# Kernel optimization log

Measured on AMD Instinct MI355X. Metric: run time of the kernel, lower is better.

## Reference

```python
import jax, jax.numpy as jnp
import numpy as np

LAYER_SIZES = [256, 256, 256]
SPLIT_HALF = True
B, F0, D = 512, 32, 32


def setup_inputs() -> dict:
    key = jax.random.key(0)
    ks = jax.random.split(key, 7)
    field_nums = [F0]
    for i, s in enumerate(LAYER_SIZES):
        field_nums.append(s // 2 if (SPLIT_HALF and i != len(LAYER_SIZES) - 1) else (s // 2 if SPLIT_HALF else s))
    # field_nums = [32, 128, 128, 128] (last entry unused for weights)
    inp = {
        'feat': jax.random.normal(ks[0], (B, F0, D), dtype=jnp.float32),
        'W0': jax.random.normal(ks[1], (LAYER_SIZES[0], field_nums[0], F0), dtype=jnp.float32) * 0.05,
        'b0': jnp.zeros((LAYER_SIZES[0],), dtype=jnp.float32),
        'W1': jax.random.normal(ks[2], (LAYER_SIZES[1], field_nums[1], F0), dtype=jnp.float32) * 0.05,
        'b1': jnp.zeros((LAYER_SIZES[1],), dtype=jnp.float32),
        'W2': jax.random.normal(ks[3], (LAYER_SIZES[2], field_nums[2], F0), dtype=jnp.float32) * 0.05,
        'b2': jnp.zeros((LAYER_SIZES[2],), dtype=jnp.float32),
    }
    return inp


def _cin_layer(h, feat, W, b):
    # h: [B,H,D], feat: [B,F0,D], W: [K,H,F0], b: [K] -> out [B,K,D]
    # outer product per embedding dim, then 1x1 conv (full [H,F0] contraction)
    z = jnp.einsum('bid,bjd->bdij', h, feat)          # [B,D,H,F0]
    out = jnp.einsum('bdij,kij->bkd', z, W) + b[None, :, None]
    return jax.nn.relu(out)


def reference(feat, W0, b0, W1, b1, W2, b2):
    Ws = [W0, W1, W2]
    bs = [b0, b1, b2]
    h = feat
    p = []
    n_layers = len(LAYER_SIZES)
    for l, K in enumerate(LAYER_SIZES):
        out = _cin_layer(h, feat, Ws[l], bs[l])        # [B,K,D]
        if SPLIT_HALF and l != n_layers - 1:
            h = out[:, :K // 2, :]
            direct = out[:, K // 2:, :]
        else:
            direct = out
            h = out
        p.append(direct)
    return jnp.concatenate(p, axis=1).sum(-1)          # [B, sum of direct sizes]
```

## Files before the change

### kernel.cpp

```cpp
#include <hip/hip_runtime.h>
#include <hip/hip_fp16.h>
#include <stdint.h>


typedef _Float16 half8_t __attribute__((ext_vector_type(8)));
typedef float f32x4 __attribute__((ext_vector_type(4)));
typedef float f32x16 __attribute__((ext_vector_type(16)));
typedef uint32_t u32x4 __attribute__((ext_vector_type(4)));

union H8 {
  half8_t h;
  uint32_t u[4];
  u32x4 q;
};

#define AS1 __attribute__((address_space(1)))
#define AS3 __attribute__((address_space(3)))

static __device__ __forceinline__ uint32_t pkmul(uint32_t x, uint32_t y) {
  __half2 a = __builtin_bit_cast(__half2, x);
  __half2 b = __builtin_bit_cast(__half2, y);
  __half2 r = __hmul2(a, b);
  return __builtin_bit_cast(uint32_t, r);
}

static __device__ __forceinline__ uint32_t pack2h(float a, float b) {
  __half2 r = __floats2half2_rn(a, b);
  return __builtin_bit_cast(uint32_t, r);
}

__global__ void prep_kernel(const float* __restrict__ W0, const float* __restrict__ W1,
                            const float* __restrict__ W2, const float* __restrict__ feat,
                            uint16_t* __restrict__ Wt0, uint16_t* __restrict__ Wt1,
                            uint16_t* __restrict__ Wt2,
                            uint16_t* __restrict__ F16, uint32_t* __restrict__ hP0) {
  int blk = blockIdx.x;
  if (blk < 1152) {
    const float* W; uint16_t* Wt; int FLsh, base;
    if (blk < 128)      { W = W0; Wt = Wt0; FLsh = 5; base = 0; }
    else if (blk < 640) { W = W1; Wt = Wt1; FLsh = 7; base = 128; }
    else                { W = W2; Wt = Wt2; FLsh = 7; base = 640; }
    int idx4 = (blk - base) * 256 + threadIdx.x;
    int jg = idx4 & 3;
    int i = (idx4 >> 2) & ((1 << FLsh) - 1);
    int k = idx4 >> (2 + FLsh);
    const float* src = W + ((size_t)(k << FLsh) + i) * 32 + jg * 8;
    float4 x0 = *(const float4*)(src);
    float4 x1 = *(const float4*)(src + 4);
    u32x4 o;
    o[0] = pack2h(x0.x, x0.y);
    o[1] = pack2h(x0.z, x0.w);
    o[2] = pack2h(x1.x, x1.y);
    o[3] = pack2h(x1.z, x1.w);
    int kr = k & 15, kt = k >> 4;
    *(u32x4*)((uint32_t*)Wt + (((size_t)i * 16 + kt) * 64 + jg * 16 + kr) * 4) = o;
  } else {
    int m = (blk - 1152) * 256 + threadIdx.x;
    int b = m >> 5, d = m & 31;
    const float* fb = feat + (size_t)b * 1024 + d;
    uint16_t hs[32];
#pragma unroll
    for (int j = 0; j < 32; ++j)
      hs[j] = __half_as_ushort(__float2half(fb[j * 32]));
    int mb = m >> 5, ml = m & 31;
#pragma unroll
    for (int jp = 0; jp < 16; ++jp) {
      uint32_t pr = (uint32_t)hs[2 * jp] | ((uint32_t)hs[2 * jp + 1] << 16);
      hP0[((size_t)(mb * 4 + (jp >> 2)) * 4 + (jp & 3)) * 32 + ml] = pr;
    }
#pragma unroll
    for (int c = 0; c < 4; ++c) {
      u32x4 q;
      q[0] = (uint32_t)hs[c * 8 + 0] | ((uint32_t)hs[c * 8 + 1] << 16);
      q[1] = (uint32_t)hs[c * 8 + 2] | ((uint32_t)hs[c * 8 + 3] << 16);
      q[2] = (uint32_t)hs[c * 8 + 4] | ((uint32_t)hs[c * 8 + 5] << 16);
      q[3] = (uint32_t)hs[c * 8 + 6] | ((uint32_t)hs[c * 8 + 7] << 16);
      *(u32x4*)(F16 + (size_t)m * 32 + c * 8) = q;
    }
  }
}

template <int FL>
__global__ __launch_bounds__(256, 2) void gemm_cin(
    const uint32_t* __restrict__ hP,
    const uint16_t* __restrict__ wt,
    const uint16_t* __restrict__ f16m,
    const float* __restrict__ bias,
    uint32_t* __restrict__ houtP,
    float* __restrict__ outp,
    int obase, int klo) {
  constexpr int NCHK = FL / 8;
  constexpr int NCM = NCHK - 1;
  __shared__ __align__(16) char smem[49152];
  const int tid = threadIdx.x;
  const int lane = tid & 63, w = tid >> 6;
  const int l31 = lane & 31, l5 = lane >> 5;
  const int kg = blockIdx.x & 7, mgrp = blockIdx.x >> 3;
  const int mb0 = mgrp * 8 + w * 2;

  const uint16_t* fb0 = f16m + (size_t)(mb0 * 32 + l31) * 32 + l5 * 8;
  H8 ffA0, ffA1, ffB0, ffB1;
  ffA0.q = *(const u32x4*)(fb0);
  ffA1.q = *(const u32x4*)(fb0 + 16);
  ffB0.q = *(const u32x4*)(fb0 + 1024);
  ffB1.q = *(const u32x4*)(fb0 + 1040);

  const char* wsrc = (const char*)wt + kg * 2048 + (size_t)(tid >> 7) * 16384 +
                     (tid & 127) * 16;
  char* sdst = smem + tid * 16;

#define STAGE(QQ, BUFOFF)                                                     \
  { const char* s_ = wsrc + (size_t)((QQ) & NCM) * 131072;                    \
    char* d_ = sdst + (BUFOFF);                                               \
    _Pragma("unroll") for (int c_ = 0; c_ < 4; ++c_)                          \
      __builtin_amdgcn_global_load_lds(                                       \
          (const AS1 uint32_t*)(s_ + c_ * 32768),                             \
          (AS3 uint32_t*)(d_ + c_ * 4096), 16, 0, 0); }

  const uint32_t* hbA = hP + (size_t)mb0 * (FL / 8) * 128 + l31;
  const uint32_t* hbB = hbA + (size_t)(FL / 8) * 128;

#define HLD(QQ, DA, DB)                                                       \
  { const uint32_t* pa_ = hbA + ((QQ) & NCM) * 128;                           \
    const uint32_t* pb_ = hbB + ((QQ) & NCM) * 128;                           \
    DA[0] = pa_[0]; DA[1] = pa_[32]; DA[2] = pa_[64]; DA[3] = pa_[96];        \
    DB[0] = pb_[0]; DB[1] = pb_[32]; DB[2] = pb_[64]; DB[3] = pb_[96]; }

  u32x4 hcA, hcB, hnA, hnB;

  STAGE(0, 0)
  STAGE(1, 16384)
  HLD(0, hcA, hcB)

  f32x16 accA0 = {}, accA1 = {}, accB0 = {}, accB1 = {};
  const char* rbase = smem + ((l31 >> 4) << 10) + (l5 << 8) + ((lane & 15) << 4);

  asm volatile("s_waitcnt vmcnt(12)" ::: "memory");
  __builtin_amdgcn_s_barrier();

#define BSTEP(HA_, HB_, PSEL, BA0, BA1, BB0, BB1)                             \
  { uint32_t eA_ = __builtin_amdgcn_perm((HA_), (HA_), (PSEL));               \
    uint32_t eB_ = __builtin_amdgcn_perm((HB_), (HB_), (PSEL));               \
    _Pragma("unroll") for (int c_ = 0; c_ < 4; ++c_) {                        \
      BA0.u[c_] = pkmul(ffA0.u[c_], eA_);                                     \
      BA1.u[c_] = pkmul(ffA1.u[c_], eA_);                                     \
      BB0.u[c_] = pkmul(ffB0.u[c_], eB_);                                     \
      BB1.u[c_] = pkmul(ffB1.u[c_], eB_);                                     \
    } }

#define MQUAD(WE, WO, BA0, BA1, BB0, BB1)                                         \
  accA0 = __builtin_amdgcn_mfma_f32_32x32x16_f16((WE).h, BA0.h, accA0, 0, 0, 0);  \
  accB0 = __builtin_amdgcn_mfma_f32_32x32x16_f16((WE).h, BB0.h, accB0, 0, 0, 0);  \
  accA1 = __builtin_amdgcn_mfma_f32_32x32x16_f16((WO).h, BA1.h, accA1, 0, 0, 0);  \
  accB1 = __builtin_amdgcn_mfma_f32_32x32x16_f16((WO).h, BB1.h, accB1, 0, 0, 0);

#define CHUNK(QQ, RDOFF, STOFF, HCA_, HCB_, HNA_, HNB_)                           \
  { const char* rb_ = rbase + (RDOFF);                                            \
    H8 w0, w1, w2, w3, w4, w5, w6, w7, w8, w9, wa, wb, wc, wd, we, wf;            \
    w0.q = *(const u32x4*)(rb_ + 0 * 2048);                                       \
    w1.q = *(const u32x4*)(rb_ + 0 * 2048 + 512);                                 \
    w2.q = *(const u32x4*)(rb_ + 1 * 2048);                                       \
    w3.q = *(const u32x4*)(rb_ + 1 * 2048 + 512);                                 \
    w4.q = *(const u32x4*)(rb_ + 2 * 2048);                                       \
    w5.q = *(const u32x4*)(rb_ + 2 * 2048 + 512);                                 \
    w6.q = *(const u32x4*)(rb_ + 3 * 2048);                                       \
    w7.q = *(const u32x4*)(rb_ + 3 * 2048 + 512);                                 \
    w8.q = *(const u32x4*)(rb_ + 4 * 2048);                                       \
    w9.q = *(const u32x4*)(rb_ + 4 * 2048 + 512);                                 \
    wa.q = *(const u32x4*)(rb_ + 5 * 2048);                                       \
    wb.q = *(const u32x4*)(rb_ + 5 * 2048 + 512);                                 \
    wc.q = *(const u32x4*)(rb_ + 6 * 2048);                                       \
    wd.q = *(const u32x4*)(rb_ + 6 * 2048 + 512);                                 \
    we.q = *(const u32x4*)(rb_ + 7 * 2048);                                       \
    wf.q = *(const u32x4*)(rb_ + 7 * 2048 + 512);                                 \
    HLD((QQ) + 1, HNA_, HNB_)                                                     \
    STAGE((QQ) + 2, STOFF)                                                        \
               \
    { H8 pA0_0, pA1_0, pB0_0, pB1_0, pA0_1, pA1_1, pB0_1, pB1_1;                  \
      H8 pA0_2, pA1_2, pB0_2, pB1_2, pA0_3, pA1_3, pB0_3, pB1_3;                  \
      BSTEP(HCA_[0], HCB_[0], 0x01000100u, pA0_0, pA1_0, pB0_0, pB1_0)            \
      BSTEP(HCA_[0], HCB_[0], 0x03020302u, pA0_1, pA1_1, pB0_1, pB1_1)            \
      BSTEP(HCA_[1], HCB_[1], 0x01000100u, pA0_2, pA1_2, pB0_2, pB1_2)            \
      BSTEP(HCA_[1], HCB_[1], 0x03020302u, pA0_3, pA1_3, pB0_3, pB1_3)            \
      __builtin_amdgcn_s_setprio(1);                                              \
      MQUAD(w0, w1, pA0_0, pA1_0, pB0_0, pB1_0)                                   \
      MQUAD(w2, w3, pA0_1, pA1_1, pB0_1, pB1_1)                                   \
      MQUAD(w4, w5, pA0_2, pA1_2, pB0_2, pB1_2)                                   \
      MQUAD(w6, w7, pA0_3, pA1_3, pB0_3, pB1_3)                                   \
      __builtin_amdgcn_s_setprio(0); }                                            \
                                                          \
    { H8 pA0_0, pA1_0, pB0_0, pB1_0, pA0_1, pA1_1, pB0_1, pB1_1;                  \
      H8 pA0_2, pA1_2, pB0_2, pB1_2, pA0_3, pA1_3, pB0_3, pB1_3;                  \
      BSTEP(HCA_[2], HCB_[2], 0x01000100u, pA0_0, pA1_0, pB0_0, pB1_0)            \
      BSTEP(HCA_[2], HCB_[2], 0x03020302u, pA0_1, pA1_1, pB0_1, pB1_1)            \
      BSTEP(HCA_[3], HCB_[3], 0x01000100u, pA0_2, pA1_2, pB0_2, pB1_2)            \
      BSTEP(HCA_[3], HCB_[3], 0x03020302u, pA0_3, pA1_3, pB0_3, pB1_3)            \
      __builtin_amdgcn_s_setprio(1);                                              \
      MQUAD(w8, w9, pA0_0, pA1_0, pB0_0, pB1_0)                                   \
      MQUAD(wa, wb, pA0_1, pA1_1, pB0_1, pB1_1)                                   \
      MQUAD(wc, wd, pA0_2, pA1_2, pB0_2, pB1_2)                                   \
      MQUAD(we, wf, pA0_3, pA1_3, pB0_3, pB1_3)                                   \
      __builtin_amdgcn_s_setprio(0); }                                            \
    asm volatile("s_waitcnt vmcnt(12)" ::: "memory");                             \
    __builtin_amdgcn_s_barrier();                                                 \
  }

  int r0 = 0, r1 = 16384, r2 = 32768;
#pragma unroll 1
  for (int q = 0; q < NCHK; q += 2) {
    CHUNK(q, r0, r2, hcA, hcB, hnA, hnB)
    CHUNK(q + 1, r1, r0, hnA, hnB, hcA, hcB)
    int t = r2; r2 = r1; r1 = r0; r0 = t;
  }
#undef CHUNK
#undef MQUAD
#undef BSTEP
#undef STAGE
#undef HLD

  asm volatile("s_waitcnt vmcnt(0)" ::: "memory");

  f32x16 accA = accA0 + accA1;
  f32x16 accB = accB0 + accB1;
  f32x4 bv[4];
#pragma unroll
  for (int a = 0; a < 4; ++a)
    bv[a] = *(const f32x4*)(bias + kg * 32 + a * 8 + l5 * 4);

#define EPILOG(ACC, MB)                                                           \
  {                                                                               \
    float v[16];                                                                  \
    _Pragma("unroll") for (int a = 0; a < 4; ++a)                                 \
        _Pragma("unroll") for (int t = 0; t < 4; ++t) {                           \
      float x = ACC[a * 4 + t] + bv[a][t];                                        \
      v[a * 4 + t] = x > 0.f ? x : 0.f;                                           \
    }                                                                             \
    if (houtP != nullptr && kg < 4) {                                             \
      _Pragma("unroll") for (int a = 0; a < 4; ++a)                               \
          _Pragma("unroll") for (int c = 0; c < 2; ++c) {                         \
        uint32_t pr = pack2h(v[a * 4 + 2 * c], v[a * 4 + 2 * c + 1]);             \
        houtP[((size_t)((MB) * 16 + kg * 4 + a) * 4 + 2 * l5 + c) * 32 + l31] =   \
            pr;                                                                   \
      }                                                                           \
    }                                                                             \
    _Pragma("unroll") for (int r = 0; r < 16; ++r) {                              \
      float x = v[r];                                                             \
      x += __shfl_xor(x, 1); x += __shfl_xor(x, 2);                               \
      x += __shfl_xor(x, 4); x += __shfl_xor(x, 8);                               \
      x += __shfl_xor(x, 16);                                                     \
      v[r] = x;                                                                   \
    }                                                                             \
    if (kg * 32 >= klo && (lane == 0 || lane == 32)) {                            \
      float* ob = outp + (size_t)(MB) * 512 + obase + kg * 32 - klo + l5 * 4;     \
      _Pragma("unroll") for (int a = 0; a < 4; ++a)                               \
          *(f32x4*)(ob + a * 8) =                                                 \
              (f32x4){v[a * 4], v[a * 4 + 1], v[a * 4 + 2], v[a * 4 + 3]};        \
    }                                                                             \
  }

  EPILOG(accA, mb0)
  EPILOG(accB, mb0 + 1)
#undef EPILOG
}

extern "C" void kernel_launch(void* const* d_in, const int* in_sizes, int n_in,
                              void* d_out, int out_size, void* d_ws, size_t ws_size,
                              hipStream_t stream) {
  const float* feat = (const float*)d_in[0];
  const float* W0 = (const float*)d_in[1];
  const float* b0 = (const float*)d_in[2];
  const float* W1 = (const float*)d_in[3];
  const float* b1 = (const float*)d_in[4];
  const float* W2 = (const float*)d_in[5];
  const float* b2 = (const float*)d_in[6];
  float* out = (float*)d_out;
  char* ws = (char*)d_ws;

  uint16_t* Wt0 = (uint16_t*)(ws + 0x000000);
  uint16_t* Wt1 = (uint16_t*)(ws + 0x080000);
  uint16_t* Wt2 = (uint16_t*)(ws + 0x280000);
  uint16_t* F16 = (uint16_t*)(ws + 0x480000);
  uint32_t* hP0 = (uint32_t*)(ws + 0x580000);
  uint32_t* hP1 = (uint32_t*)(ws + 0x680000);
  uint32_t* hP2 = (uint32_t*)(ws + 0xA80000);

  prep_kernel<<<1216, 256, 0, stream>>>(W0, W1, W2, feat, Wt0, Wt1, Wt2, F16, hP0);

  gemm_cin<32><<<512, 256, 0, stream>>>(hP0, Wt0, F16, b0, hP1, out, 0, 128);
  gemm_cin<128><<<512, 256, 0, stream>>>(hP1, Wt1, F16, b1, hP2, out, 128, 128);
  gemm_cin<128><<<512, 256, 0, stream>>>(hP2, Wt2, F16, b2, (uint32_t*)nullptr,
                                         out, 256, 0);
}
```

Measured before the change: 107.7 us.

## Software-pipeline LDS weight reads and products across half-chunks with single accumulators

Restructures the main loop into a ping-pong schedule. Weight fragments for the next half-chunk are read from LDS, and the fp16 outer-product operands are computed, while MFMAs for the current half run. It also merges the even/odd accumulator pairs into one accumulator per batch row, which frees registers but lengthens MFMA dependency chains. Barriers and vmcnt waits are reordered (wait vmcnt(0) at start, vmcnt(20) per iteration), and the extra barrier per iteration may add sync overhead.

```diff
diff --git a/kernel.cpp b/kernel.cpp
--- a/kernel.cpp
+++ b/kernel.cpp
@@ -132,10 +132,10 @@
   STAGE(1, 16384)
   HLD(0, hcA, hcB)
 
-  f32x16 accA0 = {}, accA1 = {}, accB0 = {}, accB1 = {};
+  f32x16 accA = {}, accB = {};
   const char* rbase = smem + ((l31 >> 4) << 10) + (l5 << 8) + ((lane & 15) << 4);
 
-  asm volatile("s_waitcnt vmcnt(12)" ::: "memory");
+  asm volatile("s_waitcnt vmcnt(0)" ::: "memory");
   __builtin_amdgcn_s_barrier();
 
 #define BSTEP(HA_, HB_, PSEL, BA0, BA1, BB0, BB1)                             \
@@ -148,71 +148,94 @@
       BB1.u[c_] = pkmul(ffB1.u[c_], eB_);                                     \
     } }
 
-#define MQUAD(WE, WO, BA0, BA1, BB0, BB1)                                         \
-  accA0 = __builtin_amdgcn_mfma_f32_32x32x16_f16((WE).h, BA0.h, accA0, 0, 0, 0);  \
-  accB0 = __builtin_amdgcn_mfma_f32_32x32x16_f16((WE).h, BB0.h, accB0, 0, 0, 0);  \
-  accA1 = __builtin_amdgcn_mfma_f32_32x32x16_f16((WO).h, BA1.h, accA1, 0, 0, 0);  \
-  accB1 = __builtin_amdgcn_mfma_f32_32x32x16_f16((WO).h, BB1.h, accB1, 0, 0, 0);
-
-#define CHUNK(QQ, RDOFF, STOFF, HCA_, HCB_, HNA_, HNB_)                           \
-  { const char* rb_ = rbase + (RDOFF);                                            \
-    H8 w0, w1, w2, w3, w4, w5, w6, w7, w8, w9, wa, wb, wc, wd, we, wf;            \
-    w0.q = *(const u32x4*)(rb_ + 0 * 2048);                                       \
-    w1.q = *(const u32x4*)(rb_ + 0 * 2048 + 512);                                 \
-    w2.q = *(const u32x4*)(rb_ + 1 * 2048);                                       \
-    w3.q = *(const u32x4*)(rb_ + 1 * 2048 + 512);                                 \
-    w4.q = *(const u32x4*)(rb_ + 2 * 2048);                                       \
-    w5.q = *(const u32x4*)(rb_ + 2 * 2048 + 512);                                 \
-    w6.q = *(const u32x4*)(rb_ + 3 * 2048);                                       \
-    w7.q = *(const u32x4*)(rb_ + 3 * 2048 + 512);                                 \
-    w8.q = *(const u32x4*)(rb_ + 4 * 2048);                                       \
-    w9.q = *(const u32x4*)(rb_ + 4 * 2048 + 512);                                 \
-    wa.q = *(const u32x4*)(rb_ + 5 * 2048);                                       \
-    wb.q = *(const u32x4*)(rb_ + 5 * 2048 + 512);                                 \
-    wc.q = *(const u32x4*)(rb_ + 6 * 2048);                                       \
-    wd.q = *(const u32x4*)(rb_ + 6 * 2048 + 512);                                 \
-    we.q = *(const u32x4*)(rb_ + 7 * 2048);                                       \
-    wf.q = *(const u32x4*)(rb_ + 7 * 2048 + 512);                                 \
-    HLD((QQ) + 1, HNA_, HNB_)                                                     \
-    STAGE((QQ) + 2, STOFF)                                                        \
-               \
-    { H8 pA0_0, pA1_0, pB0_0, pB1_0, pA0_1, pA1_1, pB0_1, pB1_1;                  \
-      H8 pA0_2, pA1_2, pB0_2, pB1_2, pA0_3, pA1_3, pB0_3, pB1_3;                  \
-      BSTEP(HCA_[0], HCB_[0], 0x01000100u, pA0_0, pA1_0, pB0_0, pB1_0)            \
-      BSTEP(HCA_[0], HCB_[0], 0x03020302u, pA0_1, pA1_1, pB0_1, pB1_1)            \
-      BSTEP(HCA_[1], HCB_[1], 0x01000100u, pA0_2, pA1_2, pB0_2, pB1_2)            \
-      BSTEP(HCA_[1], HCB_[1], 0x03020302u, pA0_3, pA1_3, pB0_3, pB1_3)            \
-      __builtin_amdgcn_s_setprio(1);                                              \
-      MQUAD(w0, w1, pA0_0, pA1_0, pB0_0, pB1_0)                                   \
-      MQUAD(w2, w3, pA0_1, pA1_1, pB0_1, pB1_1)                                   \
-      MQUAD(w4, w5, pA0_2, pA1_2, pB0_2, pB1_2)                                   \
-      MQUAD(w6, w7, pA0_3, pA1_3, pB0_3, pB1_3)                                   \
-      __builtin_amdgcn_s_setprio(0); }                                            \
-                                                          \
-    { H8 pA0_0, pA1_0, pB0_0, pB1_0, pA0_1, pA1_1, pB0_1, pB1_1;                  \
-      H8 pA0_2, pA1_2, pB0_2, pB1_2, pA0_3, pA1_3, pB0_3, pB1_3;                  \
-      BSTEP(HCA_[2], HCB_[2], 0x01000100u, pA0_0, pA1_0, pB0_0, pB1_0)            \
-      BSTEP(HCA_[2], HCB_[2], 0x03020302u, pA0_1, pA1_1, pB0_1, pB1_1)            \
-      BSTEP(HCA_[3], HCB_[3], 0x01000100u, pA0_2, pA1_2, pB0_2, pB1_2)            \
-      BSTEP(HCA_[3], HCB_[3], 0x03020302u, pA0_3, pA1_3, pB0_3, pB1_3)            \
-      __builtin_amdgcn_s_setprio(1);                                              \
-      MQUAD(w8, w9, pA0_0, pA1_0, pB0_0, pB1_0)                                   \
-      MQUAD(wa, wb, pA0_1, pA1_1, pB0_1, pB1_1)                                   \
-      MQUAD(wc, wd, pA0_2, pA1_2, pB0_2, pB1_2)                                   \
-      MQUAD(we, wf, pA0_3, pA1_3, pB0_3, pB1_3)                                   \
-      __builtin_amdgcn_s_setprio(0); }                                            \
-    asm volatile("s_waitcnt vmcnt(12)" ::: "memory");                             \
-    __builtin_amdgcn_s_barrier();                                                 \
+#define MQUAD(WE, WO, BA0, BA1, BB0, BB1)                                        \
+  accA = __builtin_amdgcn_mfma_f32_32x32x16_f16((WE).h, BA0.h, accA, 0, 0, 0);   \
+  accB = __builtin_amdgcn_mfma_f32_32x32x16_f16((WE).h, BB0.h, accB, 0, 0, 0);   \
+  accA = __builtin_amdgcn_mfma_f32_32x32x16_f16((WO).h, BA1.h, accA, 0, 0, 0);   \
+  accB = __builtin_amdgcn_mfma_f32_32x32x16_f16((WO).h, BB1.h, accB, 0, 0, 0);
+
+  H8 wa0, wa1, wa2, wa3, wa4, wa5, wa6, wa7;
+  H8 wb0, wb1, wb2, wb3, wb4, wb5, wb6, wb7;
+  H8 pa00, pa01, pa02, pa03, pa10, pa11, pa12, pa13;
+  H8 pa20, pa21, pa22, pa23, pa30, pa31, pa32, pa33;
+  H8 pb00, pb01, pb02, pb03, pb10, pb11, pb12, pb13;
+  H8 pb20, pb21, pb22, pb23, pb30, pb31, pb32, pb33;
+
+  {
+    const char* rb_ = rbase;
+    wa0.q = *(const u32x4*)(rb_ + 0 * 2048);
+    wa1.q = *(const u32x4*)(rb_ + 0 * 2048 + 512);
+    wa2.q = *(const u32x4*)(rb_ + 1 * 2048);
+    wa3.q = *(const u32x4*)(rb_ + 1 * 2048 + 512);
+    wa4.q = *(const u32x4*)(rb_ + 2 * 2048);
+    wa5.q = *(const u32x4*)(rb_ + 2 * 2048 + 512);
+    wa6.q = *(const u32x4*)(rb_ + 3 * 2048);
+    wa7.q = *(const u32x4*)(rb_ + 3 * 2048 + 512);
+    BSTEP(hcA[0], hcB[0], 0x01000100u, pa00, pa01, pa02, pa03)
+    BSTEP(hcA[0], hcB[0], 0x03020302u, pa10, pa11, pa12, pa13)
+    BSTEP(hcA[1], hcB[1], 0x01000100u, pa20, pa21, pa22, pa23)
+    BSTEP(hcA[1], hcB[1], 0x03020302u, pa30, pa31, pa32, pa33)
   }
 
-  int r0 = 0, r1 = 16384, r2 = 32768;
+  int c0 = 0, c1 = 16384, c2 = 32768;
 #pragma unroll 1
-  for (int q = 0; q < NCHK; q += 2) {
-    CHUNK(q, r0, r2, hcA, hcB, hnA, hnB)
-    CHUNK(q + 1, r1, r0, hnA, hnB, hcA, hcB)
-    int t = r2; r2 = r1; r1 = r0; r0 = t;
+  for (int q = 0; q < NCHK; ++q) {
+    {
+      const char* rb_ = rbase + c0;
+      wb0.q = *(const u32x4*)(rb_ + 4 * 2048);
+      wb1.q = *(const u32x4*)(rb_ + 4 * 2048 + 512);
+      wb2.q = *(const u32x4*)(rb_ + 5 * 2048);
+      wb3.q = *(const u32x4*)(rb_ + 5 * 2048 + 512);
+      wb4.q = *(const u32x4*)(rb_ + 6 * 2048);
+      wb5.q = *(const u32x4*)(rb_ + 6 * 2048 + 512);
+      wb6.q = *(const u32x4*)(rb_ + 7 * 2048);
+      wb7.q = *(const u32x4*)(rb_ + 7 * 2048 + 512);
+      HLD(q + 1, hnA, hnB)
+      BSTEP(hcA[2], hcB[2], 0x01000100u, pb00, pb01, pb02, pb03)
+      BSTEP(hcA[2], hcB[2], 0x03020302u, pb10, pb11, pb12, pb13)
+      __builtin_amdgcn_s_barrier();
+      __builtin_amdgcn_s_setprio(1);
+      MQUAD(wa0, wa1, pa00, pa01, pa02, pa03)
+      MQUAD(wa2, wa3, pa10, pa11, pa12, pa13)
+      __builtin_amdgcn_s_setprio(0);
+      BSTEP(hcA[3], hcB[3], 0x01000100u, pb20, pb21, pb22, pb23)
+      BSTEP(hcA[3], hcB[3], 0x03020302u, pb30, pb31, pb32, pb33)
+      __builtin_amdgcn_s_setprio(1);
+      MQUAD(wa4, wa5, pa20, pa21, pa22, pa23)
+      MQUAD(wa6, wa7, pa30, pa31, pa32, pa33)
+      __builtin_amdgcn_s_setprio(0);
+      __builtin_amdgcn_s_barrier();
+    }
+    {
+      STAGE(q + 2, c2)
+      asm volatile("s_waitcnt vmcnt(20)" ::: "memory");
+      __builtin_amdgcn_s_barrier();
+      const char* rb_ = rbase + c1;
+      wa0.q = *(const u32x4*)(rb_ + 0 * 2048);
+      wa1.q = *(const u32x4*)(rb_ + 0 * 2048 + 512);
+      wa2.q = *(const u32x4*)(rb_ + 1 * 2048);
+      wa3.q = *(const u32x4*)(rb_ + 1 * 2048 + 512);
+      wa4.q = *(const u32x4*)(rb_ + 2 * 2048);
+      wa5.q = *(const u32x4*)(rb_ + 2 * 2048 + 512);
+      wa6.q = *(const u32x4*)(rb_ + 3 * 2048);
+      wa7.q = *(const u32x4*)(rb_ + 3 * 2048 + 512);
+      BSTEP(hnA[0], hnB[0], 0x01000100u, pa00, pa01, pa02, pa03)
+      BSTEP(hnA[0], hnB[0], 0x03020302u, pa10, pa11, pa12, pa13)
+      __builtin_amdgcn_s_setprio(1);
+      MQUAD(wb0, wb1, pb00, pb01, pb02, pb03)
+      MQUAD(wb2, wb3, pb10, pb11, pb12, pb13)
+      __builtin_amdgcn_s_setprio(0);
+      BSTEP(hnA[1], hnB[1], 0x01000100u, pa20, pa21, pa22, pa23)
+      BSTEP(hnA[1], hnB[1], 0x03020302u, pa30, pa31, pa32, pa33)
+      __builtin_amdgcn_s_setprio(1);
+      MQUAD(wb4, wb5, pb20, pb21, pb22, pb23)
+      MQUAD(wb6, wb7, pb30, pb31, pb32, pb33)
+      __builtin_amdgcn_s_setprio(0);
+      __builtin_amdgcn_s_barrier();
+    }
+    hcA = hnA; hcB = hnB;
+    int t = c0; c0 = c1; c1 = c2; c2 = t;
   }
-#undef CHUNK
 #undef MQUAD
 #undef BSTEP
 #undef STAGE
@@ -220,8 +243,6 @@
 
   asm volatile("s_waitcnt vmcnt(0)" ::: "memory");
 
-  f32x16 accA = accA0 + accA1;
-  f32x16 accB = accB0 + accB1;
   f32x4 bv[4];
 #pragma unroll
   for (int a = 0; a < 4; ++a)
```

Measured after the change: 106.5 us. Within noise of the previous version (-1.1%).
